# Kernel tuning notes

Hardware: AMD Instinct MI355X
Metric: run time of the kernel (lower is better)

Reference implementation:

```python
import jax, jax.numpy as jnp
import numpy as np
import math

HEAD_DIM = 64
EMBED_DIM = 512
B, T = 16, 2048

def setup_inputs() -> dict:
    key = jax.random.key(0)
    k1, k2, k3 = jax.random.split(key, 3)
    x = jax.random.normal(k1, (B, T, EMBED_DIM), dtype=jnp.float32)
    # nn.Linear-style init scale
    s = 1.0 / math.sqrt(EMBED_DIM)
    Wq = jax.random.uniform(k2, (EMBED_DIM, HEAD_DIM), dtype=jnp.float32, minval=-s, maxval=s)
    bq = jax.random.uniform(k3, (HEAD_DIM,), dtype=jnp.float32, minval=-s, maxval=s)
    return {"x": x, "Wq": Wq, "bq": bq}

def reference(x, Wq, bq):
    # Faithful to source: q, k, v all come from the SAME query projection.
    q = jnp.einsum('bte,ed->btd', x, Wq) + bq  # [B,T,D]
    d_k = q.shape[-1]
    # weights[b, i, j] = q_i . q_j / sqrt(d_k)
    weights = jnp.einsum('bid,bjd->bij', q, q) / jnp.sqrt(jnp.float32(d_k))
    # NOTE: source applies softmax over dim=1 (query/row axis), not dim=-1.
    weights = jax.nn.softmax(weights, axis=1)
    attention = jnp.einsum('bij,bjd->bid', weights, q)  # v == q in source
    return attention
```

## Files before the change

kernel.cpp:

```cpp
#include <hip/hip_runtime.h>
#include <hip/hip_bf16.h>

#define BN 16
#define TN 2048
#define DN 64
#define EN 512
#define PAD 72

using f32x4  = __attribute__((ext_vector_type(4))) float;
using bf16x8 = __attribute__((ext_vector_type(8))) short;
using bf16x4 = __attribute__((ext_vector_type(4))) short;

static __device__ __forceinline__ short f2bf(float f) {
    __hip_bfloat16 h = __float2bfloat16(f);
    return __builtin_bit_cast(short, h);
}
static __device__ __forceinline__ float bf2f(short s) {
    return __bfloat162float(__builtin_bit_cast(__hip_bfloat16, s));
}

__global__ __launch_bounds__(256) void wprep_kernel(
    const float* __restrict__ Wq, short* __restrict__ WTh,
    short* __restrict__ WTl)
{
    __shared__ float wlds[64][65];
    const int tid = threadIdx.x;
    const int k0 = blockIdx.x * 64;
    #pragma unroll
    for (int it = 0; it < 16; ++it) {
        int idx = it * 256 + tid;
        int k = idx >> 6, n = idx & 63;
        wlds[k][n] = Wq[(size_t)(k0 + k) * 64 + n];
    }
    __syncthreads();
    #pragma unroll
    for (int it = 0; it < 16; ++it) {
        int idx = it * 256 + tid;
        int n = idx >> 6, k = idx & 63;
        float v = wlds[k][n];
        short h = f2bf(v);
        short l = f2bf(v - bf2f(h));
        WTh[(size_t)n * EN + k0 + k] = h;
        WTl[(size_t)n * EN + k0 + k] = l;
    }
}

__global__ __launch_bounds__(256, 2) void qproj_kernel(
    const float* __restrict__ x, const short* __restrict__ WTh,
    const short* __restrict__ WTl, const float* __restrict__ bq,
    short* __restrict__ Qb, short* __restrict__ QTb)
{
    __shared__ short xh[64 * 40];
    __shared__ short wth[64 * 40];
    __shared__ short wtl[64 * 40];
    __shared__ short tl[64][68];

    const int tid = threadIdx.x;
    const int lane = tid & 63;
    const int wv = tid >> 6;
    const int c = lane & 15;
    const int g = lane >> 4;
    const int rowbase = blockIdx.x * 64;
    const int b = rowbase >> 11;
    const int tbase = rowbase & (TN - 1);

    const int sr = tid >> 3;
    const int sc4 = tid & 7;

    float4 xa = *reinterpret_cast<const float4*>(&x[(size_t)(rowbase + sr) * EN + sc4 * 4]);
    float4 xb = *reinterpret_cast<const float4*>(&x[(size_t)(rowbase + 32 + sr) * EN + sc4 * 4]);
    bf16x4 wa = *reinterpret_cast<const bf16x4*>(&WTh[(size_t)sr * EN + sc4 * 4]);
    bf16x4 wb = *reinterpret_cast<const bf16x4*>(&WTh[(size_t)(32 + sr) * EN + sc4 * 4]);
    bf16x4 la = *reinterpret_cast<const bf16x4*>(&WTl[(size_t)sr * EN + sc4 * 4]);
    bf16x4 lb = *reinterpret_cast<const bf16x4*>(&WTl[(size_t)(32 + sr) * EN + sc4 * 4]);

    f32x4 acc[4];
    #pragma unroll
    for (int nt = 0; nt < 4; ++nt) acc[nt] = (f32x4){0.f, 0.f, 0.f, 0.f};

    for (int ks = 0; ks < EN; ks += 32) {
        __syncthreads();
        bf16x4 h0, h1;
        #pragma unroll
        for (int j = 0; j < 4; ++j) { h0[j] = f2bf(xa[j]); h1[j] = f2bf(xb[j]); }
        *reinterpret_cast<bf16x4*>(&xh[sr * 40 + sc4 * 4]) = h0;
        *reinterpret_cast<bf16x4*>(&xh[(32 + sr) * 40 + sc4 * 4]) = h1;
        *reinterpret_cast<bf16x4*>(&wth[sr * 40 + sc4 * 4]) = wa;
        *reinterpret_cast<bf16x4*>(&wth[(32 + sr) * 40 + sc4 * 4]) = wb;
        *reinterpret_cast<bf16x4*>(&wtl[sr * 40 + sc4 * 4]) = la;
        *reinterpret_cast<bf16x4*>(&wtl[(32 + sr) * 40 + sc4 * 4]) = lb;

        const int kn = (ks + 32 < EN) ? ks + 32 : ks;
        xa = *reinterpret_cast<const float4*>(&x[(size_t)(rowbase + sr) * EN + kn + sc4 * 4]);
        xb = *reinterpret_cast<const float4*>(&x[(size_t)(rowbase + 32 + sr) * EN + kn + sc4 * 4]);
        wa = *reinterpret_cast<const bf16x4*>(&WTh[(size_t)sr * EN + kn + sc4 * 4]);
        wb = *reinterpret_cast<const bf16x4*>(&WTh[(size_t)(32 + sr) * EN + kn + sc4 * 4]);
        la = *reinterpret_cast<const bf16x4*>(&WTl[(size_t)sr * EN + kn + sc4 * 4]);
        lb = *reinterpret_cast<const bf16x4*>(&WTl[(size_t)(32 + sr) * EN + kn + sc4 * 4]);
        __syncthreads();

        bf16x8 av = *reinterpret_cast<const bf16x8*>(&xh[(wv * 16 + c) * 40 + g * 8]);
        #pragma unroll
        for (int nt = 0; nt < 4; ++nt) {
            bf16x8 bh = *reinterpret_cast<const bf16x8*>(&wth[(nt * 16 + c) * 40 + g * 8]);
            bf16x8 bl = *reinterpret_cast<const bf16x8*>(&wtl[(nt * 16 + c) * 40 + g * 8]);
            acc[nt] = __builtin_amdgcn_mfma_f32_16x16x32_bf16(av, bh, acc[nt], 0, 0, 0);
            acc[nt] = __builtin_amdgcn_mfma_f32_16x16x32_bf16(av, bl, acc[nt], 0, 0, 0);
        }
    }

    __syncthreads();
    #pragma unroll
    for (int nt = 0; nt < 4; ++nt) {
        const float bias = bq[nt * 16 + c];
        #pragma unroll
        for (int r = 0; r < 4; ++r) {
            const int row = wv * 16 + g * 4 + r;
            short qb = f2bf(acc[nt][r] + bias);
            Qb[(size_t)(rowbase + row) * DN + nt * 16 + c] = qb;
            tl[nt * 16 + c][row] = qb;
        }
    }
    __syncthreads();
    #pragma unroll
    for (int it = 0; it < 4; ++it) {
        int idx = it * 256 + tid;
        int d = idx >> 4;
        int j4 = (idx & 15) * 4;
        *reinterpret_cast<short4*>(&QTb[((size_t)(b * 64 + d)) * TN + tbase + j4]) =
            *reinterpret_cast<const short4*>(&tl[d][j4]);
    }
}

__global__ __launch_bounds__(256, 2) void stats_kernel(
    const short* __restrict__ Qb, float* __restrict__ linv)
{
    __shared__ short Qt[64 * PAD];
    const int tid = threadIdx.x;
    const int lane = tid & 63;
    const int wv = tid >> 6;
    const int c = lane & 15;
    const int g = lane >> 4;
    const int b = blockIdx.y;
    const int jbase = blockIdx.x * 64 + wv * 16;
    const short* Qbb = Qb + (size_t)b * TN * DN;

    bf16x8 a0 = *reinterpret_cast<const bf16x8*>(Qbb + (size_t)(jbase + c) * DN + g * 8);
    bf16x8 a1 = *reinterpret_cast<const bf16x8*>(Qbb + (size_t)(jbase + c) * DN + g * 8 + 32);

    const int srow = tid >> 2;
    const int schk = tid & 3;

    bf16x8 v0 = *reinterpret_cast<const bf16x8*>(Qbb + (size_t)srow * DN + schk * 16);
    bf16x8 v1 = *reinterpret_cast<const bf16x8*>(Qbb + (size_t)srow * DN + schk * 16 + 8);

    float l[4] = {0.f, 0.f, 0.f, 0.f};
    for (int ib = 0; ib < TN; ib += 64) {
        __syncthreads();
        *reinterpret_cast<bf16x8*>(&Qt[srow * PAD + schk * 16]) = v0;
        *reinterpret_cast<bf16x8*>(&Qt[srow * PAD + schk * 16 + 8]) = v1;
        const int in_ = (ib + 64 < TN) ? ib + 64 : ib;
        v0 = *reinterpret_cast<const bf16x8*>(Qbb + (size_t)(in_ + srow) * DN + schk * 16);
        v1 = *reinterpret_cast<const bf16x8*>(Qbb + (size_t)(in_ + srow) * DN + schk * 16 + 8);
        __syncthreads();

        #pragma unroll
        for (int it = 0; it < 4; ++it) {
            bf16x8 b0 = *reinterpret_cast<const bf16x8*>(&Qt[(it * 16 + c) * PAD + g * 8]);
            bf16x8 b1 = *reinterpret_cast<const bf16x8*>(&Qt[(it * 16 + c) * PAD + g * 8 + 32]);
            f32x4 acc = {0.f, 0.f, 0.f, 0.f};
            acc = __builtin_amdgcn_mfma_f32_16x16x32_bf16(a0, b0, acc, 0, 0, 0);
            acc = __builtin_amdgcn_mfma_f32_16x16x32_bf16(a1, b1, acc, 0, 0, 0);
            #pragma unroll
            for (int r = 0; r < 4; ++r)
                l[r] += __expf(acc[r] * 0.125f);
        }
    }
    #pragma unroll
    for (int r = 0; r < 4; ++r) {
        float v = l[r];
        v += __shfl_xor(v, 1);
        v += __shfl_xor(v, 2);
        v += __shfl_xor(v, 4);
        v += __shfl_xor(v, 8);
        l[r] = v;
    }
    if (c == 0) {
        #pragma unroll
        for (int r = 0; r < 4; ++r)
            linv[(size_t)b * TN + jbase + g * 4 + r] = 1.0f / l[r];
    }
}

__global__ __launch_bounds__(256, 2) void pv_kernel(
    const short* __restrict__ Qb, const short* __restrict__ QTb,
    const float* __restrict__ linv, float* __restrict__ out)
{
    __shared__ short Qt[64 * PAD];
    __shared__ short QTt[64 * PAD];
    __shared__ short Pt[4][16 * PAD];
    __shared__ float lv[64];

    const int tid = threadIdx.x;
    const int lane = tid & 63;
    const int wv = tid >> 6;
    const int c = lane & 15;
    const int g = lane >> 4;
    const int b = blockIdx.y;
    const int ibase = blockIdx.x * 64 + wv * 16;
    const short* Qbb = Qb + (size_t)b * TN * DN;
    const short* QTbb = QTb + (size_t)b * DN * TN;
    const float* linvb = linv + (size_t)b * TN;

    bf16x8 bi0 = *reinterpret_cast<const bf16x8*>(Qbb + (size_t)(ibase + c) * DN + g * 8);
    bf16x8 bi1 = *reinterpret_cast<const bf16x8*>(Qbb + (size_t)(ibase + c) * DN + g * 8 + 32);

    f32x4 o[4];
    #pragma unroll
    for (int dt = 0; dt < 4; ++dt) o[dt] = (f32x4){0.f, 0.f, 0.f, 0.f};

    const int srow = tid >> 2;
    const int schk = tid & 3;

    bf16x8 vq0 = *reinterpret_cast<const bf16x8*>(Qbb + (size_t)srow * DN + schk * 16);
    bf16x8 vq1 = *reinterpret_cast<const bf16x8*>(Qbb + (size_t)srow * DN + schk * 16 + 8);
    bf16x8 vt0 = *reinterpret_cast<const bf16x8*>(QTbb + (size_t)srow * TN + schk * 16);
    bf16x8 vt1 = *reinterpret_cast<const bf16x8*>(QTbb + (size_t)srow * TN + schk * 16 + 8);
    float vl = (tid < 64) ? linvb[tid] : 0.f;

    for (int jb = 0; jb < TN; jb += 64) {
        __syncthreads();
        *reinterpret_cast<bf16x8*>(&Qt[srow * PAD + schk * 16]) = vq0;
        *reinterpret_cast<bf16x8*>(&Qt[srow * PAD + schk * 16 + 8]) = vq1;
        *reinterpret_cast<bf16x8*>(&QTt[srow * PAD + schk * 16]) = vt0;
        *reinterpret_cast<bf16x8*>(&QTt[srow * PAD + schk * 16 + 8]) = vt1;
        if (tid < 64) lv[tid] = vl;

        const int jn = (jb + 64 < TN) ? jb + 64 : jb;
        vq0 = *reinterpret_cast<const bf16x8*>(Qbb + (size_t)(jn + srow) * DN + schk * 16);
        vq1 = *reinterpret_cast<const bf16x8*>(Qbb + (size_t)(jn + srow) * DN + schk * 16 + 8);
        vt0 = *reinterpret_cast<const bf16x8*>(QTbb + (size_t)srow * TN + jn + schk * 16);
        vt1 = *reinterpret_cast<const bf16x8*>(QTbb + (size_t)srow * TN + jn + schk * 16 + 8);
        vl = (tid < 64) ? linvb[jn + tid] : 0.f;
        __syncthreads();

        #pragma unroll
        for (int jt = 0; jt < 4; ++jt) {
            bf16x8 a0 = *reinterpret_cast<const bf16x8*>(&Qt[(jt * 16 + c) * PAD + g * 8]);
            bf16x8 a1 = *reinterpret_cast<const bf16x8*>(&Qt[(jt * 16 + c) * PAD + g * 8 + 32]);
            f32x4 accs = {0.f, 0.f, 0.f, 0.f};
            accs = __builtin_amdgcn_mfma_f32_16x16x32_bf16(a0, bi0, accs, 0, 0, 0);
            accs = __builtin_amdgcn_mfma_f32_16x16x32_bf16(a1, bi1, accs, 0, 0, 0);
            f32x4 lw = *reinterpret_cast<const f32x4*>(&lv[jt * 16 + g * 4]);
            bf16x4 pw;
            #pragma unroll
            for (int r = 0; r < 4; ++r)
                pw[r] = f2bf(__expf(accs[r] * 0.125f) * lw[r]);
            *reinterpret_cast<bf16x4*>(&Pt[wv][c * PAD + jt * 16 + g * 4]) = pw;
        }
        asm volatile("s_waitcnt lgkmcnt(0)" ::: "memory");
        __builtin_amdgcn_sched_barrier(0);

        bf16x8 p0 = *reinterpret_cast<const bf16x8*>(&Pt[wv][c * PAD + g * 8]);
        bf16x8 p1 = *reinterpret_cast<const bf16x8*>(&Pt[wv][c * PAD + 32 + g * 8]);
        #pragma unroll
        for (int dt = 0; dt < 4; ++dt) {
            bf16x8 aq0 = *reinterpret_cast<const bf16x8*>(&QTt[(dt * 16 + c) * PAD + g * 8]);
            bf16x8 aq1 = *reinterpret_cast<const bf16x8*>(&QTt[(dt * 16 + c) * PAD + 32 + g * 8]);
            o[dt] = __builtin_amdgcn_mfma_f32_16x16x32_bf16(aq0, p0, o[dt], 0, 0, 0);
            o[dt] = __builtin_amdgcn_mfma_f32_16x16x32_bf16(aq1, p1, o[dt], 0, 0, 0);
        }
    }

    float* outb = out + (size_t)b * TN * DN;
    #pragma unroll
    for (int dt = 0; dt < 4; ++dt) {
        float4 v4;
        v4.x = o[dt][0]; v4.y = o[dt][1]; v4.z = o[dt][2]; v4.w = o[dt][3];
        *reinterpret_cast<float4*>(&outb[(size_t)(ibase + c) * DN + dt * 16 + g * 4]) = v4;
    }
}

extern "C" void kernel_launch(void* const* d_in, const int* in_sizes, int n_in,
                              void* d_out, int out_size, void* d_ws, size_t ws_size,
                              hipStream_t stream) {
    const float* x  = (const float*)d_in[0];
    const float* Wq = (const float*)d_in[1];
    const float* bq = (const float*)d_in[2];
    float* out = (float*)d_out;

    short* Qb  = (short*)d_ws;
    short* QTb = Qb + (size_t)BN * TN * DN;
    float* linv = (float*)(QTb + (size_t)BN * TN * DN);
    short* WTh = (short*)(linv + (size_t)BN * TN);
    short* WTl = WTh + (size_t)DN * EN;

    wprep_kernel<<<dim3(EN / 64), dim3(256), 0, stream>>>(Wq, WTh, WTl);
    qproj_kernel<<<dim3(BN * TN / 64), dim3(256), 0, stream>>>(x, WTh, WTl, bq, Qb, QTb);
    stats_kernel<<<dim3(TN / 64, BN), dim3(256), 0, stream>>>(Qb, linv);
    pv_kernel<<<dim3(TN / 64, BN), dim3(256), 0, stream>>>(Qb, QTb, linv, out);
}
```

Measured before the change: 81.23 us.

## Split attention reductions in two along sequence and fold normalizer into V

```diff
diff --git a/kernel.cpp b/kernel.cpp
--- a/kernel.cpp
+++ b/kernel.cpp
@@ -132,8 +132,8 @@
     }
 }
 
-__global__ __launch_bounds__(256, 2) void stats_kernel(
-    const short* __restrict__ Qb, float* __restrict__ linv)
+__global__ __launch_bounds__(256, 4) void stats_kernel(
+    const short* __restrict__ Qb, float* __restrict__ l_part)
 {
     __shared__ short Qt[64 * PAD];
     const int tid = threadIdx.x;
@@ -142,6 +142,7 @@
     const int c = lane & 15;
     const int g = lane >> 4;
     const int b = blockIdx.y;
+    const int z = blockIdx.z;
     const int jbase = blockIdx.x * 64 + wv * 16;
     const short* Qbb = Qb + (size_t)b * TN * DN;
 
@@ -150,16 +151,17 @@
 
     const int srow = tid >> 2;
     const int schk = tid & 3;
-
-    bf16x8 v0 = *reinterpret_cast<const bf16x8*>(Qbb + (size_t)srow * DN + schk * 16);
-    bf16x8 v1 = *reinterpret_cast<const bf16x8*>(Qbb + (size_t)srow * DN + schk * 16 + 8);
+    const int ilo = z * (TN / 2);
+
+    bf16x8 v0 = *reinterpret_cast<const bf16x8*>(Qbb + (size_t)(ilo + srow) * DN + schk * 16);
+    bf16x8 v1 = *reinterpret_cast<const bf16x8*>(Qbb + (size_t)(ilo + srow) * DN + schk * 16 + 8);
 
     float l[4] = {0.f, 0.f, 0.f, 0.f};
-    for (int ib = 0; ib < TN; ib += 64) {
+    for (int ii = 0; ii < TN / 2; ii += 64) {
         __syncthreads();
         *reinterpret_cast<bf16x8*>(&Qt[srow * PAD + schk * 16]) = v0;
         *reinterpret_cast<bf16x8*>(&Qt[srow * PAD + schk * 16 + 8]) = v1;
-        const int in_ = (ib + 64 < TN) ? ib + 64 : ib;
+        const int in_ = ilo + ((ii + 64 < TN / 2) ? ii + 64 : ii);
         v0 = *reinterpret_cast<const bf16x8*>(Qbb + (size_t)(in_ + srow) * DN + schk * 16);
         v1 = *reinterpret_cast<const bf16x8*>(Qbb + (size_t)(in_ + srow) * DN + schk * 16 + 8);
         __syncthreads();
@@ -188,18 +190,37 @@
     if (c == 0) {
         #pragma unroll
         for (int r = 0; r < 4; ++r)
-            linv[(size_t)b * TN + jbase + g * 4 + r] = 1.0f / l[r];
-    }
-}
-
-__global__ __launch_bounds__(256, 2) void pv_kernel(
-    const short* __restrict__ Qb, const short* __restrict__ QTb,
-    const float* __restrict__ linv, float* __restrict__ out)
+            l_part[((size_t)z * BN + b) * TN + jbase + g * 4 + r] = l[r];
+    }
+}
+
+__global__ __launch_bounds__(256) void fuse_kernel(
+    const short* __restrict__ QTb, const float* __restrict__ l_part,
+    short* __restrict__ RT)
+{
+    const int idx = blockIdx.x * 256 + threadIdx.x;
+    const int c8 = idx & 255;
+    const int bd = idx >> 8;
+    const int b = bd >> 6;
+    const int j0 = c8 * 8;
+
+    bf16x8 q = *reinterpret_cast<const bf16x8*>(&QTb[(size_t)bd * TN + j0]);
+    const float* lp0 = l_part + (size_t)b * TN + j0;
+    const float* lp1 = l_part + (size_t)(BN + b) * TN + j0;
+    bf16x8 r;
+    #pragma unroll
+    for (int t = 0; t < 8; ++t)
+        r[t] = f2bf(bf2f(q[t]) / (lp0[t] + lp1[t]));
+    *reinterpret_cast<bf16x8*>(&RT[(size_t)bd * TN + j0]) = r;
+}
+
+__global__ __launch_bounds__(256, 4) void pv_kernel(
+    const short* __restrict__ Qb, const short* __restrict__ RT,
+    float* __restrict__ out)
 {
     __shared__ short Qt[64 * PAD];
-    __shared__ short QTt[64 * PAD];
+    __shared__ short RTt[64 * PAD];
     __shared__ short Pt[4][16 * PAD];
-    __shared__ float lv[64];
 
     const int tid = threadIdx.x;
     const int lane = tid & 63;
@@ -207,10 +228,10 @@
     const int c = lane & 15;
     const int g = lane >> 4;
     const int b = blockIdx.y;
+    const int z = blockIdx.z;
     const int ibase = blockIdx.x * 64 + wv * 16;
     const short* Qbb = Qb + (size_t)b * TN * DN;
-    const short* QTbb = QTb + (size_t)b * DN * TN;
-    const float* linvb = linv + (size_t)b * TN;
+    const short* RTb = RT + (size_t)b * DN * TN;
 
     bf16x8 bi0 = *reinterpret_cast<const bf16x8*>(Qbb + (size_t)(ibase + c) * DN + g * 8);
     bf16x8 bi1 = *reinterpret_cast<const bf16x8*>(Qbb + (size_t)(ibase + c) * DN + g * 8 + 32);
@@ -221,28 +242,33 @@
 
     const int srow = tid >> 2;
     const int schk = tid & 3;
-
-    bf16x8 vq0 = *reinterpret_cast<const bf16x8*>(Qbb + (size_t)srow * DN + schk * 16);
-    bf16x8 vq1 = *reinterpret_cast<const bf16x8*>(Qbb + (size_t)srow * DN + schk * 16 + 8);
-    bf16x8 vt0 = *reinterpret_cast<const bf16x8*>(QTbb + (size_t)srow * TN + schk * 16);
-    bf16x8 vt1 = *reinterpret_cast<const bf16x8*>(QTbb + (size_t)srow * TN + schk * 16 + 8);
-    float vl = (tid < 64) ? linvb[tid] : 0.f;
-
-    for (int jb = 0; jb < TN; jb += 64) {
+    const int jlo = z * (TN / 2);
+
+    bf16x8 vq0 = *reinterpret_cast<const bf16x8*>(Qbb + (size_t)(jlo + srow) * DN + schk * 16);
+    bf16x8 vq1 = *reinterpret_cast<const bf16x8*>(Qbb + (size_t)(jlo + srow) * DN + schk * 16 + 8);
+    bf16x8 vt0 = *reinterpret_cast<const bf16x8*>(RTb + (size_t)srow * TN + jlo + schk * 16);
+    bf16x8 vt1 = *reinterpret_cast<const bf16x8*>(RTb + (size_t)srow * TN + jlo + schk * 16 + 8);
+
+    for (int jj = 0; jj < TN / 2; jj += 64) {
         __syncthreads();
         *reinterpret_cast<bf16x8*>(&Qt[srow * PAD + schk * 16]) = vq0;
         *reinterpret_cast<bf16x8*>(&Qt[srow * PAD + schk * 16 + 8]) = vq1;
-        *reinterpret_cast<bf16x8*>(&QTt[srow * PAD + schk * 16]) = vt0;
-        *reinterpret_cast<bf16x8*>(&QTt[srow * PAD + schk * 16 + 8]) = vt1;
-        if (tid < 64) lv[tid] = vl;
-
-        const int jn = (jb + 64 < TN) ? jb + 64 : jb;
+        *reinterpret_cast<bf16x8*>(&RTt[srow * PAD + schk * 16]) = vt0;
+        *reinterpret_cast<bf16x8*>(&RTt[srow * PAD + schk * 16 + 8]) = vt1;
+
+        const int jn = jlo + ((jj + 64 < TN / 2) ? jj + 64 : jj);
         vq0 = *reinterpret_cast<const bf16x8*>(Qbb + (size_t)(jn + srow) * DN + schk * 16);
         vq1 = *reinterpret_cast<const bf16x8*>(Qbb + (size_t)(jn + srow) * DN + schk * 16 + 8);
-        vt0 = *reinterpret_cast<const bf16x8*>(QTbb + (size_t)srow * TN + jn + schk * 16);
-        vt1 = *reinterpret_cast<const bf16x8*>(QTbb + (size_t)srow * TN + jn + schk * 16 + 8);
-        vl = (tid < 64) ? linvb[jn + tid] : 0.f;
-        __syncthreads();
+        vt0 = *reinterpret_cast<const bf16x8*>(RTb + (size_t)srow * TN + jn + schk * 16);
+        vt1 = *reinterpret_cast<const bf16x8*>(RTb + (size_t)srow * TN + jn + schk * 16 + 8);
+        __syncthreads();
+
+        bf16x8 aq[4][2];
+        #pragma unroll
+        for (int dt = 0; dt < 4; ++dt) {
+            aq[dt][0] = *reinterpret_cast<const bf16x8*>(&RTt[(dt * 16 + c) * PAD + g * 8]);
+            aq[dt][1] = *reinterpret_cast<const bf16x8*>(&RTt[(dt * 16 + c) * PAD + 32 + g * 8]);
+        }
 
         #pragma unroll
         for (int jt = 0; jt < 4; ++jt) {
@@ -251,11 +277,10 @@
             f32x4 accs = {0.f, 0.f, 0.f, 0.f};
             accs = __builtin_amdgcn_mfma_f32_16x16x32_bf16(a0, bi0, accs, 0, 0, 0);
             accs = __builtin_amdgcn_mfma_f32_16x16x32_bf16(a1, bi1, accs, 0, 0, 0);
-            f32x4 lw = *reinterpret_cast<const f32x4*>(&lv[jt * 16 + g * 4]);
             bf16x4 pw;
             #pragma unroll
             for (int r = 0; r < 4; ++r)
-                pw[r] = f2bf(__expf(accs[r] * 0.125f) * lw[r]);
+                pw[r] = f2bf(__expf(accs[r] * 0.125f));
             *reinterpret_cast<bf16x4*>(&Pt[wv][c * PAD + jt * 16 + g * 4]) = pw;
         }
         asm volatile("s_waitcnt lgkmcnt(0)" ::: "memory");
@@ -265,19 +290,17 @@
         bf16x8 p1 = *reinterpret_cast<const bf16x8*>(&Pt[wv][c * PAD + 32 + g * 8]);
         #pragma unroll
         for (int dt = 0; dt < 4; ++dt) {
-            bf16x8 aq0 = *reinterpret_cast<const bf16x8*>(&QTt[(dt * 16 + c) * PAD + g * 8]);
-            bf16x8 aq1 = *reinterpret_cast<const bf16x8*>(&QTt[(dt * 16 + c) * PAD + 32 + g * 8]);
-            o[dt] = __builtin_amdgcn_mfma_f32_16x16x32_bf16(aq0, p0, o[dt], 0, 0, 0);
-            o[dt] = __builtin_amdgcn_mfma_f32_16x16x32_bf16(aq1, p1, o[dt], 0, 0, 0);
+            o[dt] = __builtin_amdgcn_mfma_f32_16x16x32_bf16(aq[dt][0], p0, o[dt], 0, 0, 0);
+            o[dt] = __builtin_amdgcn_mfma_f32_16x16x32_bf16(aq[dt][1], p1, o[dt], 0, 0, 0);
         }
     }
 
     float* outb = out + (size_t)b * TN * DN;
     #pragma unroll
     for (int dt = 0; dt < 4; ++dt) {
-        float4 v4;
-        v4.x = o[dt][0]; v4.y = o[dt][1]; v4.z = o[dt][2]; v4.w = o[dt][3];
-        *reinterpret_cast<float4*>(&outb[(size_t)(ibase + c) * DN + dt * 16 + g * 4]) = v4;
+        #pragma unroll
+        for (int r = 0; r < 4; ++r)
+            atomicAdd(&outb[(size_t)(ibase + c) * DN + dt * 16 + g * 4 + r], o[dt][r]);
     }
 }
 
@@ -289,14 +312,17 @@
     const float* bq = (const float*)d_in[2];
     float* out = (float*)d_out;
 
-    short* Qb  = (short*)d_ws;
-    short* QTb = Qb + (size_t)BN * TN * DN;
-    float* linv = (float*)(QTb + (size_t)BN * TN * DN);
-    short* WTh = (short*)(linv + (size_t)BN * TN);
-    short* WTl = WTh + (size_t)DN * EN;
-
+    short* Qb   = (short*)d_ws;
+    short* QTb  = Qb + (size_t)BN * TN * DN;
+    short* RT   = QTb + (size_t)BN * TN * DN;
+    float* lpar = (float*)(RT + (size_t)BN * TN * DN);
+    short* WTh  = (short*)(lpar + (size_t)2 * BN * TN);
+    short* WTl  = WTh + (size_t)DN * EN;
+
+    hipMemsetAsync(out, 0, (size_t)out_size * sizeof(float), stream);
     wprep_kernel<<<dim3(EN / 64), dim3(256), 0, stream>>>(Wq, WTh, WTl);
     qproj_kernel<<<dim3(BN * TN / 64), dim3(256), 0, stream>>>(x, WTh, WTl, bq, Qb, QTb);
-    stats_kernel<<<dim3(TN / 64, BN), dim3(256), 0, stream>>>(Qb, linv);
-    pv_kernel<<<dim3(TN / 64, BN), dim3(256), 0, stream>>>(Qb, QTb, linv, out);
-}
+    stats_kernel<<<dim3(TN / 64, BN, 2), dim3(256), 0, stream>>>(Qb, lpar);
+    fuse_kernel<<<dim3(BN * DN * TN / 8 / 256), dim3(256), 0, stream>>>(QTb, lpar, RT);
+    pv_kernel<<<dim3(TN / 64, BN, 2), dim3(256), 0, stream>>>(Qb, RT, out);
+}
```

After: 115.2 us. +41.8%, slower.
